# Kernel tuning notes

Hardware: AMD Instinct MI355X
Metric: run time of the kernel (lower is better)

The kernel has to match this reference:

```python
import jax, jax.numpy as jnp
import numpy as np

NUM_STEPS = 128
UPSAMPLE_STEPS = 128
UP_SAMPLE_ITERS = 4
N_IMP = UPSAMPLE_STEPS // UP_SAMPLE_ITERS  # 32
BOUND = 1.0
NEAR = 0.2
FAR = 2.0


def sphere_sdf(pts):
    # stand-in for the learned SDF network: unit-ish sphere of radius 0.5
    return jnp.linalg.norm(pts, axis=-1) - 0.5


def clip_aabb(pts):
    return jnp.clip(pts, -BOUND, BOUND)


def sample_pdf(bins, weights, n_samples):
    # bins: [N, M], weights: [N, M-1]; deterministic (det=True) inverse-CDF sampling
    w = weights + 1e-5
    pdf = w / jnp.sum(w, -1, keepdims=True)
    cdf = jnp.cumsum(pdf, -1)
    cdf = jnp.concatenate([jnp.zeros_like(cdf[..., :1]), cdf], -1)  # [N, M]
    u = jnp.linspace(0.5 / n_samples, 1.0 - 0.5 / n_samples, n_samples, dtype=bins.dtype)
    u = jnp.broadcast_to(u, cdf.shape[:-1] + (n_samples,))
    inds = jax.vmap(lambda c, uu: jnp.searchsorted(c, uu, side='right'))(cdf, u)
    below = jnp.maximum(inds - 1, 0)
    above = jnp.minimum(inds, cdf.shape[-1] - 1)
    cdf_b = jnp.take_along_axis(cdf, below, -1)
    cdf_a = jnp.take_along_axis(cdf, above, -1)
    bins_b = jnp.take_along_axis(bins, below, -1)
    bins_a = jnp.take_along_axis(bins, above, -1)
    denom = cdf_a - cdf_b
    denom = jnp.where(denom < 1e-5, jnp.ones_like(denom), denom)
    t = (u - cdf_b) / denom
    return bins_b + t * (bins_a - bins_b)


def up_sample(z_vals, sdf, n_importance, inv_s):
    N = z_vals.shape[0]
    prev_sdf, next_sdf = sdf[:, :-1], sdf[:, 1:]
    prev_z, next_z = z_vals[:, :-1], z_vals[:, 1:]
    mid_sdf = (prev_sdf + next_sdf) * 0.5
    cos_val = (next_sdf - prev_sdf) / (next_z - prev_z + 1e-5)
    prev_cos = jnp.concatenate([jnp.zeros((N, 1), z_vals.dtype), cos_val[:, :-1]], -1)
    cos_val = jnp.minimum(prev_cos, cos_val)
    cos_val = jnp.clip(cos_val, -1000.0, 0.0)
    dist = next_z - prev_z
    prev_esti = mid_sdf - cos_val * dist * 0.5
    next_esti = mid_sdf + cos_val * dist * 0.5
    prev_cdf = jax.nn.sigmoid(prev_esti * inv_s)
    next_cdf = jax.nn.sigmoid(next_esti * inv_s)
    alpha = (prev_cdf - next_cdf + 1e-5) / (prev_cdf + 1e-5)
    trans = jnp.cumprod(jnp.concatenate([jnp.ones((N, 1), alpha.dtype), 1.0 - alpha + 1e-7], -1), -1)[:, :-1]
    weights = alpha * trans
    return sample_pdf(z_vals, weights, n_importance)


def cat_z_vals(rays_o, rays_d, z_vals, new_z_vals, sdf, last):
    z_cat = jnp.concatenate([z_vals, new_z_vals], -1)
    idx = jnp.argsort(z_cat, -1)
    z_sorted = jnp.take_along_axis(z_cat, idx, -1)
    if not last:
        pts = rays_o[:, None, :] + rays_d[:, None, :] * new_z_vals[..., :, None]
        new_sdf = sphere_sdf(clip_aabb(pts))
        sdf_cat = jnp.concatenate([sdf, new_sdf], -1)
        sdf = jnp.take_along_axis(sdf_cat, idx, -1)
    return z_sorted, sdf


def setup_inputs() -> dict:
    key = jax.random.key(0)
    k1, k2 = jax.random.split(key)
    rays_o = jax.random.normal(k1, (65536, 3), dtype=jnp.float32) * 0.1
    rays_d = jax.random.normal(k2, (65536, 3), dtype=jnp.float32)
    return {"rays_o": rays_o, "rays_d": rays_d}


def reference(rays_o, rays_d):
    rays_d = rays_d / (jnp.linalg.norm(rays_d, axis=-1, keepdims=True) + 1e-8)
    N = rays_o.shape[0]
    z_lin = jnp.linspace(0.0, 1.0, NUM_STEPS, dtype=rays_o.dtype)
    z_vals = NEAR + (FAR - NEAR) * jnp.broadcast_to(z_lin, (N, NUM_STEPS))
    pts = rays_o[:, None, :] + rays_d[:, None, :] * z_vals[..., :, None]
    sdf = sphere_sdf(clip_aabb(pts))  # [N, NUM_STEPS]
    for i in range(UP_SAMPLE_ITERS):
        new_z = up_sample(z_vals, sdf, N_IMP, 64.0 * 2.0 ** i)
        z_vals, sdf = cat_z_vals(rays_o, rays_d, z_vals, new_z, sdf,
                                 last=(i + 1 == UP_SAMPLE_ITERS))
    return z_vals  # [N, NUM_STEPS + UPSAMPLE_STEPS]
```

## Files before the change

### kernel.cpp

```cpp
#include <hip/hip_runtime.h>
#include <math.h>

#define WPB 4
#define RPB (WPB * 2)

__device__ __forceinline__ void wave_fence() {
    asm volatile("s_waitcnt lgkmcnt(0)" ::: "memory");
    __builtin_amdgcn_wave_barrier();
}

template<int CTRL, int RMASK>
__device__ __forceinline__ float dpp_f(float ident, float x) {
    return __int_as_float(__builtin_amdgcn_update_dpp(
        __float_as_int(ident), __float_as_int(x), CTRL, RMASK, 0xF, false));
}
template<int CTRL, int RMASK>
__device__ __forceinline__ int dpp_i(int ident, int x) {
    return __builtin_amdgcn_update_dpp(ident, x, CTRL, RMASK, 0xF, false);
}

__device__ __forceinline__ float scan32_mul(float x) {
    x *= dpp_f<0x111, 0xF>(1.f, x);
    x *= dpp_f<0x112, 0xF>(1.f, x);
    x *= dpp_f<0x114, 0xF>(1.f, x);
    x *= dpp_f<0x118, 0xF>(1.f, x);
    x *= dpp_f<0x142, 0xA>(1.f, x);
    return x;
}
__device__ __forceinline__ float scan32_add(float x) {
    x += dpp_f<0x111, 0xF>(0.f, x);
    x += dpp_f<0x112, 0xF>(0.f, x);
    x += dpp_f<0x114, 0xF>(0.f, x);
    x += dpp_f<0x118, 0xF>(0.f, x);
    x += dpp_f<0x142, 0xA>(0.f, x);
    return x;
}
__device__ __forceinline__ int scan32_max(int x) {
    x = max(x, dpp_i<0x111, 0xF>(-1, x));
    x = max(x, dpp_i<0x112, 0xF>(-1, x));
    x = max(x, dpp_i<0x114, 0xF>(-1, x));
    x = max(x, dpp_i<0x118, 0xF>(-1, x));
    x = max(x, dpp_i<0x142, 0xA>(-1, x));
    return x;
}
__device__ __forceinline__ float bcast31h(float x) {
    return __int_as_float(__builtin_amdgcn_ds_swizzle(__float_as_int(x), 0x03E0));
}

__device__ __forceinline__ float zof(int k) {
    return 0.2f + 1.8f * ((float)k * (1.0f / 127.0f));
}

struct Ray { float ox, oy, oz, dx, dy, dz; };

__device__ __forceinline__ float sdf_at(const Ray& rr, float t) {
    float px = fminf(fmaxf(rr.ox + rr.dx * t, -1.f), 1.f);
    float py = fminf(fmaxf(rr.oy + rr.dy * t, -1.f), 1.f);
    float pz = fminf(fmaxf(rr.oz + rr.dz * t, -1.f), 1.f);
    return sqrtf(px * px + py * py + pz * pz) - 0.5f;
}

template<int IT>
__device__ __forceinline__ void run_iter(float2* __restrict__ zs, float* __restrict__ cdf,
                                         int* __restrict__ mk, float* __restrict__ outr,
                                         const int l, const Ray rr)
{
    constexpr int  N = 128 + 32 * IT;
    constexpr int  M = N - 1;
    constexpr int  R = N / 32;
    constexpr bool LAST  = (IT == 3);
    constexpr bool FIRST = (IT == 0);
    const float c1 = -(float)(64 << IT) * 1.44269504f;
    const int k0 = l * R;

    float ez[R], es[R];
    if constexpr (FIRST) {
        #pragma unroll
        for (int r = 0; r < R; ++r) { ez[r] = zof(k0 + r); es[r] = sdf_at(rr, ez[r]); }
    } else {
        #pragma unroll
        for (int r = 0; r < R; ++r) { float2 v = zs[k0 + r]; ez[r] = v.x; es[r] = v.y; }
    }
    const float zend = dpp_f<0x130, 0xF>(0.f, ez[0]);
    const float send = dpp_f<0x130, 0xF>(0.f, es[0]);

    const float ckL = __fdividef(send - es[R - 1], zend - ez[R - 1] + 1e-5f);
    float cosp = dpp_f<0x138, 0xF>(0.f, ckL);
    cosp = (l == 0) ? 0.f : cosp;

    float q[R];
    #pragma unroll
    for (int r = 0; r < R; ++r) {
        const float zk1 = (r == R - 1) ? zend : ez[r + 1];
        const float sk1 = (r == R - 1) ? send : es[r + 1];
        const float ckr = __fdividef(sk1 - es[r], zk1 - ez[r] + 1e-5f);
        float cv = fminf(fminf(cosp, ckr), 0.0f);
        cv = fmaxf(cv, -1000.0f);
        const float mid = 0.5f * (es[r] + sk1);
        const float hd  = 0.5f * (zk1 - ez[r]);
        const float A = __builtin_amdgcn_exp2f(fminf(c1 * (mid - cv * hd), 43.0f));
        const float B = __builtin_amdgcn_exp2f(fminf(c1 * (mid + cv * hd), 43.0f));
        const float A1 = 1.0f + A, B1 = 1.0f + B;
        const float prod = A1 * B1;
        const float al = __fdividef((B - A) + 1e-5f * prod, B1 + 1e-5f * prod);
        float qr = (1.0f - al) + 1e-7f;
        if (r == R - 1) qr = (l == 31) ? 1.0f : qr;
        q[r] = qr;
        cosp = ckr;
    }

    float P = q[0];
    #pragma unroll
    for (int r = 1; r < R; ++r) P *= q[r];
    const float incP = scan32_mul(P);
    float T = dpp_f<0x138, 0xF>(1.f, incP);
    T = (l == 0) ? 1.0f : T;

    float wv[R], L = 0.f;
    #pragma unroll
    for (int r = 0; r < R; ++r) {
        const float a = (1.0f + 1e-7f) - q[r];
        float w_ = fmaf(a, T, 1e-5f);
        if (r == R - 1) w_ = (l == 31) ? 0.f : w_;
        wv[r] = w_;
        L += w_;
        T *= q[r];
    }
    const float incL = scan32_add(L);
    const float S = bcast31h(incL);
    float excL = dpp_f<0x138, 0xF>(0.f, incL);
    excL = (l == 0) ? 0.f : excL;
    const float invS = 1.0f / S;

    int cm[R];
    float run = excL;
    #pragma unroll
    for (int r = 0; r < R; ++r) {
        const float cdfv = run * invS;
        cdf[k0 + r] = cdfv;
        cm[r] = (int)ceilf(fmaf(cdfv, 32.0f, -0.5f));
        run += wv[r];
    }
    const int cmend = dpp_i<0x130, 0xF>(32, cm[0]);

    #pragma unroll
    for (int r = 0; r < R; ++r) {
        const int jlo = cm[r];
        const int jhi = (r == R - 1) ? cmend : cm[r + 1];
        bool ne = (jhi > jlo);
        if (r == R - 1) ne = ne && (l != 31);
        if (ne) mk[jlo] = k0 + r;
    }
    wave_fence();

    const int kk = scan32_max(mk[l]);
    const float cl = cdf[kk], ch = cdf[kk + 1];
    float zk, zk1;
    if constexpr (FIRST) { zk = zof(kk); zk1 = zof(kk + 1); }
    else                 { zk = zs[kk].x; zk1 = zs[kk + 1].x; }
    float denom = ch - cl;
    denom = (denom < 1e-5f) ? 1.0f : denom;
    const float u = (float)(2 * l + 1) * 0.015625f;
    const float nz = fmaf(__fdividef(u - cl, denom), zk1 - zk, zk);
    const int pos = kk + 1 + l;
    float ns = 0.f;
    if constexpr (!LAST) ns = sdf_at(rr, nz);

    if constexpr (!LAST && !FIRST) wave_fence();

    #pragma unroll
    for (int r = 0; r < R; ++r) {
        const int p = k0 + r + cm[r];
        if constexpr (LAST) { outr[p] = ez[r]; }
        else                { zs[p] = make_float2(ez[r], es[r]); }
    }
    if constexpr (LAST) { outr[pos] = nz; }
    else                { zs[pos] = make_float2(nz, ns); }

    if constexpr (!LAST) {
        mk[l] = -1;
        wave_fence();
    }
}

__global__ __launch_bounds__(WPB * 64) void neus_kernel(
    const float* __restrict__ rays_o, const float* __restrict__ rays_d,
    float* __restrict__ out, int nrays)
{
    __shared__ __align__(16) float2 zsS[RPB][224];
    __shared__ __align__(16) float  cdfS[RPB][224];
    __shared__               int    mkS[RPB][32];

    const int tid = threadIdx.x;
    const int rb  = tid >> 5;
    const int l   = tid & 31;
    const int ray = blockIdx.x * RPB + rb;
    if (ray >= nrays) return;

    float2* zs  = zsS[rb];
    float*  cdf = cdfS[rb];
    int*    mk  = mkS[rb];

    Ray rr;
    rr.ox = rays_o[ray * 3 + 0]; rr.oy = rays_o[ray * 3 + 1]; rr.oz = rays_o[ray * 3 + 2];
    float rx = rays_d[ray * 3 + 0], ry = rays_d[ray * 3 + 1], rz = rays_d[ray * 3 + 2];
    float inv = __fdividef(1.0f, sqrtf(rx * rx + ry * ry + rz * rz) + 1e-8f);
    rr.dx = rx * inv; rr.dy = ry * inv; rr.dz = rz * inv;

    mk[l] = -1;

    float* outr = out + (size_t)ray * 256;
    run_iter<0>(zs, cdf, mk, outr, l, rr);
    run_iter<1>(zs, cdf, mk, outr, l, rr);
    run_iter<2>(zs, cdf, mk, outr, l, rr);
    run_iter<3>(zs, cdf, mk, outr, l, rr);
}

extern "C" void kernel_launch(void* const* d_in, const int* in_sizes, int n_in,
                              void* d_out, int out_size, void* d_ws, size_t ws_size,
                              hipStream_t stream) {
    const float* rays_o = (const float*)d_in[0];
    const float* rays_d = (const float*)d_in[1];
    float* out = (float*)d_out;
    const int nrays = in_sizes[0] / 3;
    const int blocks = (nrays + RPB - 1) / RPB;
    neus_kernel<<<blocks, WPB * 64, 0, stream>>>(rays_o, rays_d, out, nrays);
}
```

Measured before the change: 100.9 us.

## Pack interval params per sample slot, replacing shared CDF array gathers

Instead of storing the full CDF array in LDS and gathering cdf[kk], cdf[kk+1], zs[kk], zs[kk+1] after the max-scan, each lane owning an interval writes a float4 (cdf low, cdf high, z, dz) into a per-sample slot and packs (k<<5)|slot into the marker. After the scan, one float4 load per lane replaces four scattered loads. The mk reset moves before the scatter writes, so one wave fence per iteration is removed. LDS use shrinks, at the cost of more stores in the marking loop.

```diff
diff --git a/kernel.cpp b/kernel.cpp
--- a/kernel.cpp
+++ b/kernel.cpp
@@ -61,12 +61,11 @@
 }
 
 template<int IT>
-__device__ __forceinline__ void run_iter(float2* __restrict__ zs, float* __restrict__ cdf,
-                                         int* __restrict__ mk, float* __restrict__ outr,
+__device__ __forceinline__ void run_iter(float2* __restrict__ zs, int* __restrict__ mk,
+                                         float4* __restrict__ pl, float* __restrict__ outr,
                                          const int l, const Ray rr)
 {
     constexpr int  N = 128 + 32 * IT;
-    constexpr int  M = N - 1;
     constexpr int  R = N / 32;
     constexpr bool LAST  = (IT == 3);
     constexpr bool FIRST = (IT == 0);
@@ -132,16 +131,17 @@
     excL = (l == 0) ? 0.f : excL;
     const float invS = 1.0f / S;
 
-    int cm[R];
+    float ce[R];
+    int   cm[R];
     float run = excL;
     #pragma unroll
     for (int r = 0; r < R; ++r) {
-        const float cdfv = run * invS;
-        cdf[k0 + r] = cdfv;
-        cm[r] = (int)ceilf(fmaf(cdfv, 32.0f, -0.5f));
+        ce[r] = run * invS;
+        cm[r] = (int)ceilf(fmaf(ce[r], 32.0f, -0.5f));
         run += wv[r];
     }
-    const int cmend = dpp_i<0x130, 0xF>(32, cm[0]);
+    const int   cmend  = dpp_i<0x130, 0xF>(32, cm[0]);
+    const float cdfend = dpp_f<0x130, 0xF>(1.f, ce[0]);
 
     #pragma unroll
     for (int r = 0; r < R; ++r) {
@@ -149,25 +149,31 @@
         const int jhi = (r == R - 1) ? cmend : cm[r + 1];
         bool ne = (jhi > jlo);
         if (r == R - 1) ne = ne && (l != 31);
-        if (ne) mk[jlo] = k0 + r;
+        if (ne) {
+            const int   k   = k0 + r;
+            const float cl  = ce[r];
+            const float ch  = (r == R - 1) ? cdfend : ce[r + 1];
+            const float zk  = ez[r];
+            const float zk1 = (r == R - 1) ? zend : ez[r + 1];
+            mk[jlo] = (k << 5) | jlo;
+            pl[jlo] = make_float4(cl, ch, zk, zk1 - zk);
+        }
     }
     wave_fence();
 
-    const int kk = scan32_max(mk[l]);
-    const float cl = cdf[kk], ch = cdf[kk + 1];
-    float zk, zk1;
-    if constexpr (FIRST) { zk = zof(kk); zk1 = zof(kk + 1); }
-    else                 { zk = zs[kk].x; zk1 = zs[kk + 1].x; }
-    float denom = ch - cl;
+    int m0 = mk[l];
+    if constexpr (!LAST) mk[l] = -1;
+    const int pack = scan32_max(m0);
+    const int kk = pack >> 5, js = pack & 31;
+    const float4 p4 = pl[js];
+    float denom = p4.y - p4.x;
     denom = (denom < 1e-5f) ? 1.0f : denom;
     const float u = (float)(2 * l + 1) * 0.015625f;
-    const float nz = fmaf(__fdividef(u - cl, denom), zk1 - zk, zk);
+    const float nz = fmaf(__fdividef(u - p4.x, denom), p4.w, p4.z);
     const int pos = kk + 1 + l;
     float ns = 0.f;
     if constexpr (!LAST) ns = sdf_at(rr, nz);
 
-    if constexpr (!LAST && !FIRST) wave_fence();
-
     #pragma unroll
     for (int r = 0; r < R; ++r) {
         const int p = k0 + r + cm[r];
@@ -177,10 +183,7 @@
     if constexpr (LAST) { outr[pos] = nz; }
     else                { zs[pos] = make_float2(nz, ns); }
 
-    if constexpr (!LAST) {
-        mk[l] = -1;
-        wave_fence();
-    }
+    if constexpr (!LAST) wave_fence();
 }
 
 __global__ __launch_bounds__(WPB * 64) void neus_kernel(
@@ -188,7 +191,7 @@
     float* __restrict__ out, int nrays)
 {
     __shared__ __align__(16) float2 zsS[RPB][224];
-    __shared__ __align__(16) float  cdfS[RPB][224];
+    __shared__ __align__(16) float4 plS[RPB][32];
     __shared__               int    mkS[RPB][32];
 
     const int tid = threadIdx.x;
@@ -197,9 +200,9 @@
     const int ray = blockIdx.x * RPB + rb;
     if (ray >= nrays) return;
 
-    float2* zs  = zsS[rb];
-    float*  cdf = cdfS[rb];
-    int*    mk  = mkS[rb];
+    float2* zs = zsS[rb];
+    float4* pl = plS[rb];
+    int*    mk = mkS[rb];
 
     Ray rr;
     rr.ox = rays_o[ray * 3 + 0]; rr.oy = rays_o[ray * 3 + 1]; rr.oz = rays_o[ray * 3 + 2];
@@ -210,10 +213,10 @@
     mk[l] = -1;
 
     float* outr = out + (size_t)ray * 256;
-    run_iter<0>(zs, cdf, mk, outr, l, rr);
-    run_iter<1>(zs, cdf, mk, outr, l, rr);
-    run_iter<2>(zs, cdf, mk, outr, l, rr);
-    run_iter<3>(zs, cdf, mk, outr, l, rr);
+    run_iter<0>(zs, mk, pl, outr, l, rr);
+    run_iter<1>(zs, mk, pl, outr, l, rr);
+    run_iter<2>(zs, mk, pl, outr, l, rr);
+    run_iter<3>(zs, mk, pl, outr, l, rr);
 }
 
 extern "C" void kernel_launch(void* const* d_in, const int* in_sizes, int n_in,
```

Result: no change. 101.4 us (+0.5%).
